# Optimization experiments

Measured on AMD Instinct MI355X. Metric: run time of the kernel, lower is better.

Reference implementation:

```python
import jax, jax.numpy as jnp
import numpy as np

N, C, H, K, HID = 131072, 256, 8, 128, 1024
SCALE = (C // H) ** -0.5  # 1/sqrt(32)


def layernorm(x, g, b, eps=1e-5):
    mu = jnp.mean(x, axis=-1, keepdims=True)
    var = jnp.var(x, axis=-1, keepdims=True)
    return (x - mu) * jax.lax.rsqrt(var + eps) * g + b


def setup_inputs() -> dict:
    key = jax.random.key(0)
    ks = jax.random.split(key, 8)
    feat = jax.random.normal(ks[0], (N, C), dtype=jnp.float32)
    order = jax.random.permutation(ks[1], N)  # serialized order (gather)
    inverse = jnp.argsort(order)              # scatter back (unpad identity)
    s = 0.02
    return {
        "feat": feat,
        "ln1_g": jnp.ones((C,), jnp.float32), "ln1_b": jnp.zeros((C,), jnp.float32),
        "w_qkv": jax.random.normal(ks[2], (C, 3 * C), jnp.float32) * s,
        "b_qkv": jnp.zeros((3 * C,), jnp.float32),
        "w_proj": jax.random.normal(ks[3], (C, C), jnp.float32) * s,
        "b_proj": jnp.zeros((C,), jnp.float32),
        "ln2_g": jnp.ones((C,), jnp.float32), "ln2_b": jnp.zeros((C,), jnp.float32),
        "w1": jax.random.normal(ks[4], (C, HID), jnp.float32) * s,
        "b1": jnp.zeros((HID,), jnp.float32),
        "w2": jax.random.normal(ks[5], (HID, C), jnp.float32) * s,
        "b2": jnp.zeros((C,), jnp.float32),
        "order": order,
        "inverse": inverse,
    }


def attention(x, w_qkv, b_qkv, w_proj, b_proj, order, inverse):
    D = C // H
    qkv = x @ w_qkv + b_qkv                       # [N, 3C]
    qkv = qkv[order]                              # gather to serialized order
    qkv = qkv.reshape(-1, K, 3, H, D)             # [P, K, 3, H, D]
    q, k, v = jnp.moveaxis(qkv, 2, 0)             # each [P, K, H, D]
    q = jnp.swapaxes(q, 1, 2)                     # [P, H, K, D]
    k = jnp.swapaxes(k, 1, 2)
    v = jnp.swapaxes(v, 1, 2)
    attn = jnp.einsum("phkd,phjd->phkj", q * SCALE, k)  # [P, H, K, K]
    attn = jax.nn.softmax(attn, axis=-1)
    out = jnp.einsum("phkj,phjd->phkd", attn, v)  # [P, H, K, D]
    out = jnp.swapaxes(out, 1, 2).reshape(-1, C)  # [N, C]
    out = out[inverse]                            # scatter back to input order
    return out @ w_proj + b_proj


def reference(feat, ln1_g, ln1_b, w_qkv, b_qkv, w_proj, b_proj,
              ln2_g, ln2_b, w1, b1, w2, b2, order, inverse):
    # pre-norm transformer block: x + attn(ln1(x)); x + mlp(ln2(x))
    x = feat
    x = x + attention(layernorm(x, ln1_g, ln1_b), w_qkv, b_qkv, w_proj, b_proj, order, inverse)
    h = layernorm(x, ln2_g, ln2_b)
    h = jax.nn.gelu(h @ w1 + b1) @ w2 + b2
    return x + h
```

## Files before the change

### kernel.cpp

```cpp
#include <hip/hip_runtime.h>
#include <hip/hip_bf16.h>

typedef __hip_bfloat16 bf16;
typedef __bf16 bf16x8 __attribute__((ext_vector_type(8)));
typedef float f32x4 __attribute__((ext_vector_type(4)));

#define N_TOK 131072
#define C_DIM 256
#define HID_DIM 1024

__device__ __forceinline__ void async_copy16(void* lds, const void* g) {
  __builtin_amdgcn_global_load_lds(
      (const __attribute__((address_space(1))) void*)g,
      (__attribute__((address_space(3))) void*)lds, 16, 0, 0);
}

__device__ __forceinline__ float fast_rcp(float x) {
#if __has_builtin(__builtin_amdgcn_rcpf)
  return __builtin_amdgcn_rcpf(x);
#else
  return 1.f / x;
#endif
}

__device__ __forceinline__ bf16 bf16_rne(float f) {
  unsigned u = __float_as_uint(f);
  u += 0x7FFF + ((u >> 16) & 1);
  unsigned short s = (unsigned short)(u >> 16);
  return *reinterpret_cast<bf16*>(&s);
}

__device__ __forceinline__ unsigned cvt_pk_bf16(float lo, float hi) {
  unsigned r;
  asm("v_cvt_pk_bf16_f32 %0, %1, %2" : "=v"(r) : "v"(lo), "v"(hi));
  return r;
}

__device__ __forceinline__ float fast_gelu(float x) {
  float t = x * x;
  float u = __builtin_fmaf(-0.10294365856f, t, -2.30220842764f);
  float z = x * u;
#if __has_builtin(__builtin_amdgcn_exp2f)
  float e = __builtin_amdgcn_exp2f(z);
#else
  float e = __expf(z * 0.69314718056f);
#endif
  return x * fast_rcp(1.f + e);
}

__global__ void ln_bf16_kernel(const float* __restrict__ x,
                               const float* __restrict__ g,
                               const float* __restrict__ b,
                               bf16* __restrict__ out) {
  int row = blockIdx.x * 4 + threadIdx.y;
  int lane = threadIdx.x;
  size_t base = (size_t)row * C_DIM + lane * 4;
  float4 v = *(const float4*)(x + base);
  float s = v.x + v.y + v.z + v.w;
  float s2 = v.x * v.x + v.y * v.y + v.z * v.z + v.w * v.w;
#pragma unroll
  for (int m = 1; m < 64; m <<= 1) { s += __shfl_xor(s, m); s2 += __shfl_xor(s2, m); }
  float mean = s * (1.f / 256.f);
  float var = s2 * (1.f / 256.f) - mean * mean;
  float rstd = rsqrtf(var + 1e-5f);
  float4 gv = *(const float4*)(g + lane * 4);
  float4 bv = *(const float4*)(b + lane * 4);
  uint2 pk;
  pk.x = cvt_pk_bf16((v.x - mean) * rstd * gv.x + bv.x,
                     (v.y - mean) * rstd * gv.y + bv.y);
  pk.y = cvt_pk_bf16((v.z - mean) * rstd * gv.z + bv.z,
                     (v.w - mean) * rstd * gv.w + bv.w);
  *(uint2*)(out + base) = pk;
}

__global__ void cast_transpose_kernel(const float* __restrict__ in, bf16* __restrict__ out,
                                      int K, int N) {
  int idx = blockIdx.x * 256 + threadIdx.x;
  if (idx >= K * N) return;
  int n = idx / K, k = idx - n * K;
  out[idx] = bf16_rne(in[(size_t)k * N + n]);
}

template <int EPI, int NXT>
__global__ __launch_bounds__(256) void gemm_bt_kernel(
    const bf16* __restrict__ A, const bf16* __restrict__ Bt,
    const float* __restrict__ bias, const float* __restrict__ res,
    void* __restrict__ outp, int K, int ldn) {
  __shared__ bf16 sA[2][128 * 64];
  __shared__ bf16 sB[2][128 * 64];
  const int bid = blockIdx.x;
  const int xcd = bid & 7;
  const int j = bid >> 3;
  const int n0 = (j % NXT) * 128;
  const int m0 = ((j / NXT) * 8 + xcd) * 128;
  const int tid = threadIdx.x;
  const int wid = tid >> 6;
  const int lane = tid & 63;
  const int quad = lane >> 4;
  const int l16 = lane & 15;
  const int wm = (wid >> 1) * 64;
  const int wn = (wid & 1) * 64;
  const int srow = tid >> 3;
  const int scol = ((tid & 7) ^ (srow & 7)) * 8;

  const bf16* pA = A + (size_t)(m0 + srow) * K + scol;
  const bf16* pB = Bt + (size_t)(n0 + srow) * K + scol;
  const size_t isStride = (size_t)32 * K;

  f32x4 acc[4][4] = {};
  const int NT = K >> 6;

#pragma unroll
  for (int is = 0; is < 4; ++is) {
    async_copy16(&sA[0][is * 2048 + wid * 512], pA + is * isStride);
    async_copy16(&sB[0][is * 2048 + wid * 512], pB + is * isStride);
  }
  pA += 64;
  pB += 64;
  __syncthreads();

  for (int t = 0; t < NT; ++t) {
    const int cur = t & 1;
    if (t + 1 < NT) {
#pragma unroll
      for (int is = 0; is < 4; ++is) {
        async_copy16(&sA[cur ^ 1][is * 2048 + wid * 512], pA + is * isStride);
        async_copy16(&sB[cur ^ 1][is * 2048 + wid * 512], pB + is * isStride);
      }
      pA += 64;
      pB += 64;
    }
    const bf16* bufA = sA[cur];
    const bf16* bufB = sB[cur];
#pragma unroll
    for (int kk = 0; kk < 64; kk += 32) {
      bf16x8 af[4], bfr[4];
#pragma unroll
      for (int i = 0; i < 4; ++i)
        af[i] = *(const bf16x8*)&bufA[(wm + i * 16 + l16) * 64 +
                                      ((((kk >> 3) + quad) ^ (l16 & 7)) << 3)];
#pragma unroll
      for (int j2 = 0; j2 < 4; ++j2)
        bfr[j2] = *(const bf16x8*)&bufB[(wn + j2 * 16 + l16) * 64 +
                                        ((((kk >> 3) + quad) ^ (l16 & 7)) << 3)];
#pragma unroll
      for (int i = 0; i < 4; ++i)
#pragma unroll
        for (int j2 = 0; j2 < 4; ++j2)
          acc[i][j2] = __builtin_amdgcn_mfma_f32_16x16x32_bf16(af[i], bfr[j2], acc[i][j2], 0, 0, 0);
    }
    __syncthreads();
  }

  float bv[4];
#pragma unroll
  for (int j2 = 0; j2 < 4; ++j2) bv[j2] = bias[n0 + wn + j2 * 16 + l16];
  const int colb = n0 + wn + l16;
#pragma unroll
  for (int i = 0; i < 4; ++i) {
    int rowb = m0 + wm + i * 16 + quad * 4;
#pragma unroll
    for (int r = 0; r < 4; ++r) {
      size_t rowoff = (size_t)(rowb + r) * ldn + colb;
#pragma unroll
      for (int j2 = 0; j2 < 4; ++j2) {
        size_t idx = rowoff + j2 * 16;
        float v = acc[i][j2][r] + bv[j2];
        if constexpr (EPI == 0) {
          ((bf16*)outp)[idx] = bf16_rne(v);
        } else if constexpr (EPI == 1) {
          ((float*)outp)[idx] = v + res[idx];
        } else if constexpr (EPI == 2) {
          ((bf16*)outp)[idx] = bf16_rne(fast_gelu(v));
        } else {
          ((float*)outp)[idx] = v + res[idx];
        }
      }
    }
  }
}

__global__ __launch_bounds__(256) void attn_kernel(
    const bf16* __restrict__ qkv, const int* __restrict__ order,
    bf16* __restrict__ outw) {
  __shared__ bf16 sK[128 * 40];
  __shared__ bf16 sVt[32 * 136];
  __shared__ bf16 sP[128 * 136];
  __shared__ int sOrd[128];
  const int bid = blockIdx.x;
  const int h = (bid >> 3) & 7;
  const int p = ((bid >> 6) << 3) | (bid & 7);
  const int tid = threadIdx.x;
  const int wid = tid >> 6;
  const int lane = tid & 63;
  const int quad = lane >> 4;
  const int l16 = lane & 15;

  if (tid < 128) sOrd[tid] = order[p * 128 + tid];
  __syncthreads();

  {
    int r = tid >> 1;
    int half = (tid & 1) * 16;
    size_t base = (size_t)sOrd[r] * 768 + h * 32;
    uint4 ka = *(const uint4*)&qkv[base + 256 + half];
    uint4 kb = *(const uint4*)&qkv[base + 256 + half + 8];
    *(uint4*)&sK[r * 40 + half] = ka;
    *(uint4*)&sK[r * 40 + half + 8] = kb;
    union { uint4 u[2]; bf16 e[16]; } vv;
    vv.u[0] = *(const uint4*)&qkv[base + 512 + half];
    vv.u[1] = *(const uint4*)&qkv[base + 512 + half + 8];
#pragma unroll
    for (int c = 0; c < 16; ++c) sVt[(half + c) * 136 + r] = vv.e[c];
  }
  __syncthreads();

  bf16x8 qf[2];
#pragma unroll
  for (int t = 0; t < 2; ++t) {
    int r = wid * 32 + t * 16 + l16;
    qf[t] = *(const bf16x8*)&qkv[(size_t)sOrd[r] * 768 + h * 32 + quad * 8];
  }

  const f32x4 zero = {0.f, 0.f, 0.f, 0.f};
  f32x4 s[2][8];
#pragma unroll
  for (int ct = 0; ct < 8; ++ct) {
    bf16x8 kf = *(const bf16x8*)&sK[(ct * 16 + l16) * 40 + quad * 8];
#pragma unroll
    for (int t = 0; t < 2; ++t)
      s[t][ct] = __builtin_amdgcn_mfma_f32_16x16x32_bf16(qf[t], kf, zero, 0, 0, 0);
  }

  const float scale = 0.17677669529663687f;
#pragma unroll
  for (int t = 0; t < 2; ++t) {
#pragma unroll
    for (int r = 0; r < 4; ++r) {
      float mx = -1e30f;
#pragma unroll
      for (int ct = 0; ct < 8; ++ct) mx = fmaxf(mx, s[t][ct][r]);
      mx *= scale;
#pragma unroll
      for (int mk = 1; mk < 16; mk <<= 1) mx = fmaxf(mx, __shfl_xor(mx, mk));
      float sum = 0.f;
#pragma unroll
      for (int ct = 0; ct < 8; ++ct) {
        float e = __expf(scale * s[t][ct][r] - mx);
        s[t][ct][r] = e;
        sum += e;
      }
#pragma unroll
      for (int mk = 1; mk < 16; mk <<= 1) sum += __shfl_xor(sum, mk);
      float inv = fast_rcp(sum);
      int prow = wid * 32 + t * 16 + quad * 4 + r;
#pragma unroll
      for (int ct = 0; ct < 8; ++ct)
        sP[prow * 136 + ct * 16 + l16] = bf16_rne(s[t][ct][r] * inv);
    }
  }
  __syncthreads();

  f32x4 o[2][2] = {};
#pragma unroll
  for (int ks = 0; ks < 4; ++ks) {
    bf16x8 vf[2];
#pragma unroll
    for (int n = 0; n < 2; ++n)
      vf[n] = *(const bf16x8*)&sVt[(n * 16 + l16) * 136 + ks * 32 + quad * 8];
#pragma unroll
    for (int t = 0; t < 2; ++t) {
      bf16x8 pf = *(const bf16x8*)&sP[(wid * 32 + t * 16 + l16) * 136 + ks * 32 + quad * 8];
#pragma unroll
      for (int n = 0; n < 2; ++n)
        o[t][n] = __builtin_amdgcn_mfma_f32_16x16x32_bf16(pf, vf[n], o[t][n], 0, 0, 0);
    }
  }

#pragma unroll
  for (int t = 0; t < 2; ++t) {
    int rowb = wid * 32 + t * 16 + quad * 4;
#pragma unroll
    for (int r = 0; r < 4; ++r) {
      size_t gbase = (size_t)sOrd[rowb + r] * 256 + h * 32;
#pragma unroll
      for (int n = 0; n < 2; ++n)
        outw[gbase + n * 16 + l16] = bf16_rne(o[t][n][r]);
    }
  }
}

extern "C" void kernel_launch(void* const* d_in, const int* in_sizes, int n_in,
                              void* d_out, int out_size, void* d_ws, size_t ws_size,
                              hipStream_t stream) {
  const float* feat   = (const float*)d_in[0];
  const float* ln1_g  = (const float*)d_in[1];
  const float* ln1_b  = (const float*)d_in[2];
  const float* w_qkv  = (const float*)d_in[3];
  const float* b_qkv  = (const float*)d_in[4];
  const float* w_proj = (const float*)d_in[5];
  const float* b_proj = (const float*)d_in[6];
  const float* ln2_g  = (const float*)d_in[7];
  const float* ln2_b  = (const float*)d_in[8];
  const float* w1     = (const float*)d_in[9];
  const float* b1     = (const float*)d_in[10];
  const float* w2     = (const float*)d_in[11];
  const float* b2     = (const float*)d_in[12];
  const int* order    = (const int*)d_in[13];
  float* out = (float*)d_out;

  char* ws = (char*)d_ws;
  size_t off = 0;
  auto take = [&](size_t bytes) {
    char* pp = ws + off;
    off += (bytes + 255) & ~(size_t)255;
    return pp;
  };
  bf16* ln_buf  = (bf16*)take((size_t)N_TOK * 256 * 2);
  bf16* qkv     = (bf16*)take((size_t)N_TOK * 768 * 2);
  bf16* attn_o  = (bf16*)take((size_t)N_TOK * 256 * 2);
  float* xres   = (float*)take((size_t)N_TOK * 256 * 4);
  bf16* wqkvT   = (bf16*)take(768 * 256 * 2);
  bf16* wprojT  = (bf16*)take(256 * 256 * 2);
  bf16* w1T     = (bf16*)take(1024 * 256 * 2);
  bf16* w2T     = (bf16*)take(256 * 1024 * 2);
  bf16* hbuf    = qkv;

  cast_transpose_kernel<<<768, 256, 0, stream>>>(w_qkv, wqkvT, 256, 768);
  cast_transpose_kernel<<<256, 256, 0, stream>>>(w_proj, wprojT, 256, 256);
  cast_transpose_kernel<<<1024, 256, 0, stream>>>(w1, w1T, 256, 1024);
  cast_transpose_kernel<<<1024, 256, 0, stream>>>(w2, w2T, 1024, 256);

  ln_bf16_kernel<<<N_TOK / 4, dim3(64, 4), 0, stream>>>(feat, ln1_g, ln1_b, ln_buf);
  gemm_bt_kernel<0, 6><<<6 * 1024, 256, 0, stream>>>(ln_buf, wqkvT, b_qkv, nullptr, qkv, 256, 768);
  attn_kernel<<<8 * 1024, 256, 0, stream>>>(qkv, order, attn_o);
  gemm_bt_kernel<1, 2><<<2 * 1024, 256, 0, stream>>>(attn_o, wprojT, b_proj, feat, xres, 256, 256);
  ln_bf16_kernel<<<N_TOK / 4, dim3(64, 4), 0, stream>>>(xres, ln2_g, ln2_b, ln_buf);
  gemm_bt_kernel<2, 8><<<8 * 1024, 256, 0, stream>>>(ln_buf, w1T, b1, nullptr, hbuf, 256, 1024);
  gemm_bt_kernel<3, 2><<<2 * 1024, 256, 0, stream>>>(hbuf, w2T, b2, xres, out, 1024, 256);
}
```

Before: 846.2 us.

## Make GEMM kernel persistent with single-buffered LDS and cross-tile prefetch

Launches a fixed 1024 blocks per GEMM that loop over output tiles with a stride, instead of one block per tile. LDS staging goes from double to single buffering. The next tile's first K-slice is prefetched so its load overlaps the epilogue. The aim is to cut block launch overhead and LDS footprint, at the cost of losing load/compute overlap within a tile's K loop.

Result: slower. 1.017 ms (+20.1%).

```diff
diff --git a/kernel.cpp b/kernel.cpp
--- a/kernel.cpp
+++ b/kernel.cpp
@@ -86,13 +86,11 @@
     const bf16* __restrict__ A, const bf16* __restrict__ Bt,
     const float* __restrict__ bias, const float* __restrict__ res,
     void* __restrict__ outp, int K, int ldn) {
-  __shared__ bf16 sA[2][128 * 64];
-  __shared__ bf16 sB[2][128 * 64];
+  __shared__ bf16 sA[128 * 64];
+  __shared__ bf16 sB[128 * 64];
   const int bid = blockIdx.x;
   const int xcd = bid & 7;
-  const int j = bid >> 3;
-  const int n0 = (j % NXT) * 128;
-  const int m0 = ((j / NXT) * 8 + xcd) * 128;
+  const int sb = bid >> 3;
   const int tid = threadIdx.x;
   const int wid = tid >> 6;
   const int lane = tid & 63;
@@ -102,78 +100,84 @@
   const int wn = (wid & 1) * 64;
   const int srow = tid >> 3;
   const int scol = ((tid & 7) ^ (srow & 7)) * 8;
-
-  const bf16* pA = A + (size_t)(m0 + srow) * K + scol;
-  const bf16* pB = Bt + (size_t)(n0 + srow) * K + scol;
   const size_t isStride = (size_t)32 * K;
-
-  f32x4 acc[4][4] = {};
   const int NT = K >> 6;
-
-#pragma unroll
-  for (int is = 0; is < 4; ++is) {
-    async_copy16(&sA[0][is * 2048 + wid * 512], pA + is * isStride);
-    async_copy16(&sB[0][is * 2048 + wid * 512], pB + is * isStride);
-  }
-  pA += 64;
-  pB += 64;
-  __syncthreads();
-
-  for (int t = 0; t < NT; ++t) {
-    const int cur = t & 1;
-    if (t + 1 < NT) {
-#pragma unroll
-      for (int is = 0; is < 4; ++is) {
-        async_copy16(&sA[cur ^ 1][is * 2048 + wid * 512], pA + is * isStride);
-        async_copy16(&sB[cur ^ 1][is * 2048 + wid * 512], pB + is * isStride);
+  const int TT = 128 * NXT;
+
+  const bf16* pA;
+  const bf16* pB;
+  int m0, n0;
+  auto setTile = [&](int t) {
+    int ml = t / NXT;
+    int nt = t - ml * NXT;
+    m0 = (ml * 8 + xcd) * 128;
+    n0 = nt * 128;
+    pA = A + (size_t)(m0 + srow) * K + scol;
+    pB = Bt + (size_t)(n0 + srow) * K + scol;
+  };
+  auto stage = [&](int s) {
+#pragma unroll
+    for (int is = 0; is < 4; ++is) {
+      async_copy16(&sA[is * 2048 + wid * 512], pA + s * 64 + is * isStride);
+      async_copy16(&sB[is * 2048 + wid * 512], pB + s * 64 + is * isStride);
+    }
+  };
+
+  int t = sb;
+  if (t < TT) { setTile(t); stage(0); }
+  for (; t < TT; t += 128) {
+    const int em0 = m0, en0 = n0;
+    f32x4 acc[4][4] = {};
+    for (int s = 0; s < NT; ++s) {
+      __syncthreads();
+#pragma unroll
+      for (int kk = 0; kk < 64; kk += 32) {
+        bf16x8 af[4], bfr[4];
+#pragma unroll
+        for (int i = 0; i < 4; ++i)
+          af[i] = *(const bf16x8*)&sA[(wm + i * 16 + l16) * 64 +
+                                      ((((kk >> 3) + quad) ^ (l16 & 7)) << 3)];
+#pragma unroll
+        for (int j2 = 0; j2 < 4; ++j2)
+          bfr[j2] = *(const bf16x8*)&sB[(wn + j2 * 16 + l16) * 64 +
+                                        ((((kk >> 3) + quad) ^ (l16 & 7)) << 3)];
+#pragma unroll
+        for (int i = 0; i < 4; ++i)
+#pragma unroll
+          for (int j2 = 0; j2 < 4; ++j2)
+            acc[i][j2] = __builtin_amdgcn_mfma_f32_16x16x32_bf16(af[i], bfr[j2], acc[i][j2], 0, 0, 0);
       }
-      pA += 64;
-      pB += 64;
-    }
-    const bf16* bufA = sA[cur];
-    const bf16* bufB = sB[cur];
-#pragma unroll
-    for (int kk = 0; kk < 64; kk += 32) {
-      bf16x8 af[4], bfr[4];
-#pragma unroll
-      for (int i = 0; i < 4; ++i)
-        af[i] = *(const bf16x8*)&bufA[(wm + i * 16 + l16) * 64 +
-                                      ((((kk >> 3) + quad) ^ (l16 & 7)) << 3)];
-#pragma unroll
-      for (int j2 = 0; j2 < 4; ++j2)
-        bfr[j2] = *(const bf16x8*)&bufB[(wn + j2 * 16 + l16) * 64 +
-                                        ((((kk >> 3) + quad) ^ (l16 & 7)) << 3)];
-#pragma unroll
-      for (int i = 0; i < 4; ++i)
-#pragma unroll
-        for (int j2 = 0; j2 < 4; ++j2)
-          acc[i][j2] = __builtin_amdgcn_mfma_f32_16x16x32_bf16(af[i], bfr[j2], acc[i][j2], 0, 0, 0);
-    }
-    __syncthreads();
-  }
-
-  float bv[4];
-#pragma unroll
-  for (int j2 = 0; j2 < 4; ++j2) bv[j2] = bias[n0 + wn + j2 * 16 + l16];
-  const int colb = n0 + wn + l16;
-#pragma unroll
-  for (int i = 0; i < 4; ++i) {
-    int rowb = m0 + wm + i * 16 + quad * 4;
-#pragma unroll
-    for (int r = 0; r < 4; ++r) {
-      size_t rowoff = (size_t)(rowb + r) * ldn + colb;
-#pragma unroll
-      for (int j2 = 0; j2 < 4; ++j2) {
-        size_t idx = rowoff + j2 * 16;
-        float v = acc[i][j2][r] + bv[j2];
-        if constexpr (EPI == 0) {
-          ((bf16*)outp)[idx] = bf16_rne(v);
-        } else if constexpr (EPI == 1) {
-          ((float*)outp)[idx] = v + res[idx];
-        } else if constexpr (EPI == 2) {
-          ((bf16*)outp)[idx] = bf16_rne(fast_gelu(v));
-        } else {
-          ((float*)outp)[idx] = v + res[idx];
+      __syncthreads();
+      if (s + 1 < NT) {
+        stage(s + 1);
+      } else if (t + 128 < TT) {
+        setTile(t + 128);
+        stage(0);
+      }
+    }
+    float bv[4];
+#pragma unroll
+    for (int j2 = 0; j2 < 4; ++j2) bv[j2] = bias[en0 + wn + j2 * 16 + l16];
+    const int colb = en0 + wn + l16;
+#pragma unroll
+    for (int i = 0; i < 4; ++i) {
+      int rowb = em0 + wm + i * 16 + quad * 4;
+#pragma unroll
+      for (int r = 0; r < 4; ++r) {
+        size_t rowoff = (size_t)(rowb + r) * ldn + colb;
+#pragma unroll
+        for (int j2 = 0; j2 < 4; ++j2) {
+          size_t idx = rowoff + j2 * 16;
+          float v = acc[i][j2][r] + bv[j2];
+          if constexpr (EPI == 0) {
+            ((bf16*)outp)[idx] = bf16_rne(v);
+          } else if constexpr (EPI == 1) {
+            ((float*)outp)[idx] = v + res[idx];
+          } else if constexpr (EPI == 2) {
+            ((bf16*)outp)[idx] = bf16_rne(fast_gelu(v));
+          } else {
+            ((float*)outp)[idx] = v + res[idx];
+          }
         }
       }
     }
@@ -332,10 +336,10 @@
   cast_transpose_kernel<<<1024, 256, 0, stream>>>(w2, w2T, 1024, 256);
 
   ln_bf16_kernel<<<N_TOK / 4, dim3(64, 4), 0, stream>>>(feat, ln1_g, ln1_b, ln_buf);
-  gemm_bt_kernel<0, 6><<<6 * 1024, 256, 0, stream>>>(ln_buf, wqkvT, b_qkv, nullptr, qkv, 256, 768);
+  gemm_bt_kernel<0, 6><<<1024, 256, 0, stream>>>(ln_buf, wqkvT, b_qkv, nullptr, qkv, 256, 768);
   attn_kernel<<<8 * 1024, 256, 0, stream>>>(qkv, order, attn_o);
-  gemm_bt_kernel<1, 2><<<2 * 1024, 256, 0, stream>>>(attn_o, wprojT, b_proj, feat, xres, 256, 256);
+  gemm_bt_kernel<1, 2><<<1024, 256, 0, stream>>>(attn_o, wprojT, b_proj, feat, xres, 256, 256);
   ln_bf16_kernel<<<N_TOK / 4, dim3(64, 4), 0, stream>>>(xres, ln2_g, ln2_b, ln_buf);
-  gemm_bt_kernel<2, 8><<<8 * 1024, 256, 0, stream>>>(ln_buf, w1T, b1, nullptr, hbuf, 256, 1024);
-  gemm_bt_kernel<3, 2><<<2 * 1024, 256, 0, stream>>>(hbuf, w2T, b2, xres, out, 1024, 256);
-}
+  gemm_bt_kernel<2, 8><<<1024, 256, 0, stream>>>(ln_buf, w1T, b1, nullptr, hbuf, 256, 1024);
+  gemm_bt_kernel<3, 2><<<1024, 256, 0, stream>>>(hbuf, w2T, b2, xres, out, 1024, 256);
+}
```

## Fuse MLP GEMMs with GELU into one kernel and single-buffer GEMM tiles

Applied to the files above, without the earlier changes.

Adds a fused MLP kernel. For each 64-row tile it computes the first GEMM in 64-wide hidden chunks, applies bias and GELU, stages the result as bf16 in LDS, and accumulates the second GEMM directly. This removes the round trip of the N×1024 hidden activation through global memory and one kernel launch. The cost is that the fused kernel reads weight fragments straight from global memory (L2) without LDS staging and uses smaller per-wave MFMA tiles for the first GEMM. Separately, the generic GEMM drops its LDS double buffering for a single buffer, which frees LDS but exposes load latency in the remaining GEMMs.

New measurement: 954.0 us. 1.13x slower.

```diff
diff --git a/kernel.cpp b/kernel.cpp
--- a/kernel.cpp
+++ b/kernel.cpp
@@ -86,8 +86,8 @@
     const bf16* __restrict__ A, const bf16* __restrict__ Bt,
     const float* __restrict__ bias, const float* __restrict__ res,
     void* __restrict__ outp, int K, int ldn) {
-  __shared__ bf16 sA[2][128 * 64];
-  __shared__ bf16 sB[2][128 * 64];
+  __shared__ bf16 sA[128 * 64];
+  __shared__ bf16 sB[128 * 64];
   const int bid = blockIdx.x;
   const int xcd = bid & 7;
   const int j = bid >> 3;
@@ -108,41 +108,27 @@
   const size_t isStride = (size_t)32 * K;
 
   f32x4 acc[4][4] = {};
-  const int NT = K >> 6;
-
-#pragma unroll
-  for (int is = 0; is < 4; ++is) {
-    async_copy16(&sA[0][is * 2048 + wid * 512], pA + is * isStride);
-    async_copy16(&sB[0][is * 2048 + wid * 512], pB + is * isStride);
-  }
-  pA += 64;
-  pB += 64;
-  __syncthreads();
-
-  for (int t = 0; t < NT; ++t) {
-    const int cur = t & 1;
-    if (t + 1 < NT) {
-#pragma unroll
-      for (int is = 0; is < 4; ++is) {
-        async_copy16(&sA[cur ^ 1][is * 2048 + wid * 512], pA + is * isStride);
-        async_copy16(&sB[cur ^ 1][is * 2048 + wid * 512], pB + is * isStride);
-      }
-      pA += 64;
-      pB += 64;
-    }
-    const bf16* bufA = sA[cur];
-    const bf16* bufB = sB[cur];
+
+  for (int k0 = 0; k0 < K; k0 += 64) {
+#pragma unroll
+    for (int is = 0; is < 4; ++is) {
+      async_copy16(&sA[is * 2048 + wid * 512], pA + is * isStride);
+      async_copy16(&sB[is * 2048 + wid * 512], pB + is * isStride);
+    }
+    pA += 64;
+    pB += 64;
+    __syncthreads();
 #pragma unroll
     for (int kk = 0; kk < 64; kk += 32) {
       bf16x8 af[4], bfr[4];
 #pragma unroll
       for (int i = 0; i < 4; ++i)
-        af[i] = *(const bf16x8*)&bufA[(wm + i * 16 + l16) * 64 +
+        af[i] = *(const bf16x8*)&sA[(wm + i * 16 + l16) * 64 +
+                                    ((((kk >> 3) + quad) ^ (l16 & 7)) << 3)];
+#pragma unroll
+      for (int j2 = 0; j2 < 4; ++j2)
+        bfr[j2] = *(const bf16x8*)&sB[(wn + j2 * 16 + l16) * 64 +
                                       ((((kk >> 3) + quad) ^ (l16 & 7)) << 3)];
-#pragma unroll
-      for (int j2 = 0; j2 < 4; ++j2)
-        bfr[j2] = *(const bf16x8*)&bufB[(wn + j2 * 16 + l16) * 64 +
-                                        ((((kk >> 3) + quad) ^ (l16 & 7)) << 3)];
 #pragma unroll
       for (int i = 0; i < 4; ++i)
 #pragma unroll
@@ -168,13 +154,114 @@
         float v = acc[i][j2][r] + bv[j2];
         if constexpr (EPI == 0) {
           ((bf16*)outp)[idx] = bf16_rne(v);
-        } else if constexpr (EPI == 1) {
-          ((float*)outp)[idx] = v + res[idx];
-        } else if constexpr (EPI == 2) {
-          ((bf16*)outp)[idx] = bf16_rne(fast_gelu(v));
         } else {
           ((float*)outp)[idx] = v + res[idx];
         }
+      }
+    }
+  }
+}
+
+__global__ __launch_bounds__(256) void mlp_fused_kernel(
+    const bf16* __restrict__ lnb, const bf16* __restrict__ w1T,
+    const bf16* __restrict__ w2T, const float* __restrict__ b1,
+    const float* __restrict__ b2, const float* __restrict__ res,
+    float* __restrict__ out) {
+  __shared__ bf16 sA[64 * 256];
+  __shared__ bf16 sH[2][64 * 64];
+  const int tid = threadIdx.x;
+  const int wid = tid >> 6;
+  const int lane = tid & 63;
+  const int quad = lane >> 4;
+  const int l16 = lane & 15;
+  const int m0 = blockIdx.x * 64;
+  const int wr = wid >> 1, wc = wid & 1;
+
+  {
+    const int row = tid >> 5;
+    const int pcb = tid & 31;
+    const bf16* pA = lnb + (size_t)(m0 + row) * 256 + ((pcb ^ row) << 3);
+#pragma unroll
+    for (int s = 0; s < 8; ++s)
+      async_copy16(&sA[s * 2048 + wid * 512], pA + s * 2048);
+  }
+  __syncthreads();
+
+  f32x4 acc2[4][4] = {};
+
+#pragma unroll 1
+  for (int hk = 0; hk < 16; ++hk) {
+    f32x4 acc1[2][2] = {};
+    const bf16* pW1 = w1T + (size_t)(hk * 64) * 256;
+#pragma unroll
+    for (int kk = 0; kk < 256; kk += 32) {
+      const int swz = ((((kk >> 3) + quad) ^ (l16 & 7)) << 3);
+      bf16x8 a1[2], bf1[2];
+#pragma unroll
+      for (int i = 0; i < 2; ++i)
+        a1[i] = *(const bf16x8*)&sA[(wr * 32 + i * 16 + l16) * 256 + swz];
+#pragma unroll
+      for (int j = 0; j < 2; ++j)
+        bf1[j] = *(const bf16x8*)&pW1[(size_t)(wc * 32 + j * 16 + l16) * 256 + kk + quad * 8];
+#pragma unroll
+      for (int i = 0; i < 2; ++i)
+#pragma unroll
+        for (int j = 0; j < 2; ++j)
+          acc1[i][j] = __builtin_amdgcn_mfma_f32_16x16x32_bf16(a1[i], bf1[j], acc1[i][j], 0, 0, 0);
+    }
+    bf16* sHb = sH[hk & 1];
+    float bv1[2];
+#pragma unroll
+    for (int j = 0; j < 2; ++j) bv1[j] = b1[hk * 64 + wc * 32 + j * 16 + l16];
+#pragma unroll
+    for (int i = 0; i < 2; ++i) {
+      const int hrow = wr * 32 + i * 16 + quad * 4;
+#pragma unroll
+      for (int r = 0; r < 4; ++r) {
+        const int rw = hrow + r;
+        const int rsw = (rw & 7) << 3;
+#pragma unroll
+        for (int j = 0; j < 2; ++j) {
+          const int hcol = wc * 32 + j * 16 + l16;
+          const float v = fast_gelu(acc1[i][j][r] + bv1[j]);
+          sHb[rw * 64 + ((hcol & 0x38) ^ rsw) + (hcol & 7)] = bf16_rne(v);
+        }
+      }
+    }
+    __syncthreads();
+    const bf16* pW2 = w2T + (size_t)hk * 64;
+#pragma unroll
+    for (int kk = 0; kk < 64; kk += 32) {
+      const int swz = ((((kk >> 3) + quad) ^ (l16 & 7)) << 3);
+      bf16x8 a2[4], bf2[4];
+#pragma unroll
+      for (int i = 0; i < 4; ++i)
+        a2[i] = *(const bf16x8*)&sHb[(i * 16 + l16) * 64 + swz];
+#pragma unroll
+      for (int j2 = 0; j2 < 4; ++j2)
+        bf2[j2] = *(const bf16x8*)&pW2[(size_t)(wid * 64 + j2 * 16 + l16) * 1024 + kk + quad * 8];
+#pragma unroll
+      for (int i = 0; i < 4; ++i)
+#pragma unroll
+        for (int j2 = 0; j2 < 4; ++j2)
+          acc2[i][j2] = __builtin_amdgcn_mfma_f32_16x16x32_bf16(a2[i], bf2[j2], acc2[i][j2], 0, 0, 0);
+    }
+  }
+
+  float bv2[4];
+#pragma unroll
+  for (int j2 = 0; j2 < 4; ++j2) bv2[j2] = b2[wid * 64 + j2 * 16 + l16];
+  const int colb = wid * 64 + l16;
+#pragma unroll
+  for (int i = 0; i < 4; ++i) {
+    const int rowb = m0 + i * 16 + quad * 4;
+#pragma unroll
+    for (int r = 0; r < 4; ++r) {
+      size_t rowoff = (size_t)(rowb + r) * 256 + colb;
+#pragma unroll
+      for (int j2 = 0; j2 < 4; ++j2) {
+        size_t idx = rowoff + j2 * 16;
+        out[idx] = acc2[i][j2][r] + bv2[j2] + res[idx];
       }
     }
   }
@@ -324,7 +411,6 @@
   bf16* wprojT  = (bf16*)take(256 * 256 * 2);
   bf16* w1T     = (bf16*)take(1024 * 256 * 2);
   bf16* w2T     = (bf16*)take(256 * 1024 * 2);
-  bf16* hbuf    = qkv;
 
   cast_transpose_kernel<<<768, 256, 0, stream>>>(w_qkv, wqkvT, 256, 768);
   cast_transpose_kernel<<<256, 256, 0, stream>>>(w_proj, wprojT, 256, 256);
@@ -336,6 +422,5 @@
   attn_kernel<<<8 * 1024, 256, 0, stream>>>(qkv, order, attn_o);
   gemm_bt_kernel<1, 2><<<2 * 1024, 256, 0, stream>>>(attn_o, wprojT, b_proj, feat, xres, 256, 256);
   ln_bf16_kernel<<<N_TOK / 4, dim3(64, 4), 0, stream>>>(xres, ln2_g, ln2_b, ln_buf);
-  gemm_bt_kernel<2, 8><<<8 * 1024, 256, 0, stream>>>(ln_buf, w1T, b1, nullptr, hbuf, 256, 1024);
-  gemm_bt_kernel<3, 2><<<2 * 1024, 256, 0, stream>>>(hbuf, w2T, b2, xres, out, 1024, 256);
-}
+  mlp_fused_kernel<<<N_TOK / 64, 256, 0, stream>>>(ln_buf, w1T, w2T, b1, b2, xres, out);
+}
```

## Pack bf16 GEMM stores via column permutation and drop LDS double buffering

Applied to the files above, without the earlier changes.

The bf16 GEMM epilogues now write pairs of adjacent values as one 32-bit store. To make that possible, output columns are permuted within each 32-wide group. The permutation is undone by permuting the K rows of w_proj and w2 during the weight cast. For qkv it relies on q and k being permuted identically within each head, and on v's permutation flowing through attention unchanged. The GEMM main loop also switches from a double-buffered LDS pipeline to a single buffer. That halves LDS use, which may allow more resident blocks, but it loses the overlap of global loads with MFMA work.

New measurement: 831.3 us. No clear change (-1.8%).

```diff
diff --git a/kernel.cpp b/kernel.cpp
--- a/kernel.cpp
+++ b/kernel.cpp
@@ -73,12 +73,15 @@
   *(uint2*)(out + base) = pk;
 }
 
+template <int PERM>
 __global__ void cast_transpose_kernel(const float* __restrict__ in, bf16* __restrict__ out,
                                       int K, int N) {
   int idx = blockIdx.x * 256 + threadIdx.x;
   if (idx >= K * N) return;
   int n = idx / K, k = idx - n * K;
-  out[idx] = bf16_rne(in[(size_t)k * N + n]);
+  int ks = k;
+  if constexpr (PERM) ks = (k & ~31) | (((k & 1) << 4) | ((k >> 1) & 15));
+  out[idx] = bf16_rne(in[(size_t)ks * N + n]);
 }
 
 template <int EPI, int NXT>
@@ -86,8 +89,8 @@
     const bf16* __restrict__ A, const bf16* __restrict__ Bt,
     const float* __restrict__ bias, const float* __restrict__ res,
     void* __restrict__ outp, int K, int ldn) {
-  __shared__ bf16 sA[2][128 * 64];
-  __shared__ bf16 sB[2][128 * 64];
+  __shared__ bf16 sA[128 * 64];
+  __shared__ bf16 sB[128 * 64];
   const int bid = blockIdx.x;
   const int xcd = bid & 7;
   const int j = bid >> 3;
@@ -108,41 +111,27 @@
   const size_t isStride = (size_t)32 * K;
 
   f32x4 acc[4][4] = {};
-  const int NT = K >> 6;
-
-#pragma unroll
-  for (int is = 0; is < 4; ++is) {
-    async_copy16(&sA[0][is * 2048 + wid * 512], pA + is * isStride);
-    async_copy16(&sB[0][is * 2048 + wid * 512], pB + is * isStride);
-  }
-  pA += 64;
-  pB += 64;
-  __syncthreads();
-
-  for (int t = 0; t < NT; ++t) {
-    const int cur = t & 1;
-    if (t + 1 < NT) {
-#pragma unroll
-      for (int is = 0; is < 4; ++is) {
-        async_copy16(&sA[cur ^ 1][is * 2048 + wid * 512], pA + is * isStride);
-        async_copy16(&sB[cur ^ 1][is * 2048 + wid * 512], pB + is * isStride);
-      }
-      pA += 64;
-      pB += 64;
-    }
-    const bf16* bufA = sA[cur];
-    const bf16* bufB = sB[cur];
+
+  for (int k0 = 0; k0 < K; k0 += 64) {
+#pragma unroll
+    for (int is = 0; is < 4; ++is) {
+      async_copy16(&sA[is * 2048 + wid * 512], pA + is * isStride);
+      async_copy16(&sB[is * 2048 + wid * 512], pB + is * isStride);
+    }
+    pA += 64;
+    pB += 64;
+    __syncthreads();
 #pragma unroll
     for (int kk = 0; kk < 64; kk += 32) {
       bf16x8 af[4], bfr[4];
 #pragma unroll
       for (int i = 0; i < 4; ++i)
-        af[i] = *(const bf16x8*)&bufA[(wm + i * 16 + l16) * 64 +
+        af[i] = *(const bf16x8*)&sA[(wm + i * 16 + l16) * 64 +
+                                    ((((kk >> 3) + quad) ^ (l16 & 7)) << 3)];
+#pragma unroll
+      for (int j2 = 0; j2 < 4; ++j2)
+        bfr[j2] = *(const bf16x8*)&sB[(wn + j2 * 16 + l16) * 64 +
                                       ((((kk >> 3) + quad) ^ (l16 & 7)) << 3)];
-#pragma unroll
-      for (int j2 = 0; j2 < 4; ++j2)
-        bfr[j2] = *(const bf16x8*)&bufB[(wn + j2 * 16 + l16) * 64 +
-                                        ((((kk >> 3) + quad) ^ (l16 & 7)) << 3)];
 #pragma unroll
       for (int i = 0; i < 4; ++i)
 #pragma unroll
@@ -155,25 +144,38 @@
   float bv[4];
 #pragma unroll
   for (int j2 = 0; j2 < 4; ++j2) bv[j2] = bias[n0 + wn + j2 * 16 + l16];
-  const int colb = n0 + wn + l16;
-#pragma unroll
-  for (int i = 0; i < 4; ++i) {
-    int rowb = m0 + wm + i * 16 + quad * 4;
-#pragma unroll
-    for (int r = 0; r < 4; ++r) {
-      size_t rowoff = (size_t)(rowb + r) * ldn + colb;
-#pragma unroll
-      for (int j2 = 0; j2 < 4; ++j2) {
-        size_t idx = rowoff + j2 * 16;
-        float v = acc[i][j2][r] + bv[j2];
-        if constexpr (EPI == 0) {
-          ((bf16*)outp)[idx] = bf16_rne(v);
-        } else if constexpr (EPI == 1) {
-          ((float*)outp)[idx] = v + res[idx];
-        } else if constexpr (EPI == 2) {
-          ((bf16*)outp)[idx] = bf16_rne(fast_gelu(v));
-        } else {
-          ((float*)outp)[idx] = v + res[idx];
+  if constexpr (EPI == 0 || EPI == 2) {
+    const int colp = n0 + wn + 2 * l16;
+#pragma unroll
+    for (int i = 0; i < 4; ++i) {
+      int rowb = m0 + wm + i * 16 + quad * 4;
+#pragma unroll
+      for (int r = 0; r < 4; ++r) {
+        float v0 = acc[i][0][r] + bv[0];
+        float v1 = acc[i][1][r] + bv[1];
+        float v2 = acc[i][2][r] + bv[2];
+        float v3 = acc[i][3][r] + bv[3];
+        if constexpr (EPI == 2) {
+          v0 = fast_gelu(v0); v1 = fast_gelu(v1);
+          v2 = fast_gelu(v2); v3 = fast_gelu(v3);
+        }
+        size_t base = (size_t)(rowb + r) * ldn + colp;
+        *(unsigned*)((bf16*)outp + base) = cvt_pk_bf16(v0, v1);
+        *(unsigned*)((bf16*)outp + base + 32) = cvt_pk_bf16(v2, v3);
+      }
+    }
+  } else {
+    const int colb = n0 + wn + l16;
+#pragma unroll
+    for (int i = 0; i < 4; ++i) {
+      int rowb = m0 + wm + i * 16 + quad * 4;
+#pragma unroll
+      for (int r = 0; r < 4; ++r) {
+        size_t rowoff = (size_t)(rowb + r) * ldn + colb;
+#pragma unroll
+        for (int j2 = 0; j2 < 4; ++j2) {
+          size_t idx = rowoff + j2 * 16;
+          ((float*)outp)[idx] = acc[i][j2][r] + bv[j2] + res[idx];
         }
       }
     }
@@ -326,10 +328,10 @@
   bf16* w2T     = (bf16*)take(256 * 1024 * 2);
   bf16* hbuf    = qkv;
 
-  cast_transpose_kernel<<<768, 256, 0, stream>>>(w_qkv, wqkvT, 256, 768);
-  cast_transpose_kernel<<<256, 256, 0, stream>>>(w_proj, wprojT, 256, 256);
-  cast_transpose_kernel<<<1024, 256, 0, stream>>>(w1, w1T, 256, 1024);
-  cast_transpose_kernel<<<1024, 256, 0, stream>>>(w2, w2T, 1024, 256);
+  cast_transpose_kernel<0><<<768, 256, 0, stream>>>(w_qkv, wqkvT, 256, 768);
+  cast_transpose_kernel<1><<<256, 256, 0, stream>>>(w_proj, wprojT, 256, 256);
+  cast_transpose_kernel<0><<<1024, 256, 0, stream>>>(w1, w1T, 256, 1024);
+  cast_transpose_kernel<1><<<1024, 256, 0, stream>>>(w2, w2T, 1024, 256);
 
   ln_bf16_kernel<<<N_TOK / 4, dim3(64, 4), 0, stream>>>(feat, ln1_g, ln1_b, ln_buf);
   gemm_bt_kernel<0, 6><<<6 * 1024, 256, 0, stream>>>(ln_buf, wqkvT, b_qkv, nullptr, qkv, 256, 768);
```
